# Optimization experiments

Hardware: AMD Instinct MI355X
Metric: run time of the kernel (lower is better)

The kernel has to match this reference:

```python
import jax, jax.numpy as jnp
import numpy as np

B, T, DIN = 1024, 256, 128
UNITS, OUT = 512, 64
INTER, CMD, MOTOR = 269, 179, 64  # AutoNCP(512, 64) layer split
SENS_FANOUT, INTER_FANOUT, MOTOR_FANIN = 134, 89, 89
LAYER_DIMS = [(DIN, INTER), (INTER, CMD), (CMD, MOTOR)]


def _layer_mask(rng, n_in, n_h, fanout=None, fanin=None):
    # sparse prev-layer -> layer block, dense recurrent block (ncps WiredCfCCell)
    m = np.zeros((n_in, n_h), dtype=bool)
    if fanout is not None:
        for i in range(n_in):
            m[i, rng.choice(n_h, size=fanout, replace=False)] = True
    else:
        for j in range(n_h):
            m[rng.choice(n_in, size=fanin, replace=False), j] = True
    full = np.concatenate([m, np.ones((n_h, n_h), dtype=bool)], axis=0)
    return jnp.asarray(full.T)  # (n_h, n_in + n_h): Linear weight layout


def setup_inputs() -> dict:
    key = jax.random.key(0)
    ks = jax.random.split(key, 30)
    rng = np.random.RandomState(22222)
    d = {}
    d["x"] = jax.random.normal(ks[0], (B, T, DIN), dtype=jnp.float32)
    d["hidden"] = jnp.zeros((B, UNITS), dtype=jnp.float32)
    d["mask0"] = _layer_mask(rng, DIN, INTER, fanout=SENS_FANOUT)
    d["mask1"] = _layer_mask(rng, INTER, CMD, fanout=INTER_FANOUT)
    d["mask2"] = _layer_mask(rng, CMD, MOTOR, fanin=MOTOR_FANIN)
    ki = 1
    for li, (n_in, n_h) in enumerate(LAYER_DIMS):
        cat = n_in + n_h
        s = 1.0 / float(np.sqrt(cat))
        for nm in ("ff1", "ff2", "ta", "tb"):
            d[f"{nm}_w{li}"] = jax.random.uniform(ks[ki], (n_h, cat), minval=-s, maxval=s, dtype=jnp.float32); ki += 1
            d[f"{nm}_b{li}"] = jax.random.uniform(ks[ki], (n_h,), minval=-s, maxval=s, dtype=jnp.float32); ki += 1
    sf = 1.0 / float(np.sqrt(MOTOR))
    d["fc_w"] = jax.random.uniform(ks[ki], (OUT, MOTOR), minval=-sf, maxval=sf, dtype=jnp.float32)
    d["fc_b"] = jax.random.uniform(ks[ki + 1], (OUT,), minval=-sf, maxval=sf, dtype=jnp.float32)
    return d


def _cfc_cell(inp, h, w1, b1, w2, b2, wa, ba, wb, bb):
    xc = jnp.concatenate([inp, h], axis=-1)
    ff1 = jnp.tanh(xc @ w1.T + b1)
    ff2 = jnp.tanh(xc @ w2.T + b2)
    ts = 1.0  # default elapsed time in CfC when no timespans given
    t_interp = jax.nn.sigmoid((xc @ wa.T + ba) * ts + (xc @ wb.T + bb))
    return ff1 * (1.0 - t_interp) + t_interp * ff2


def reference(x, hidden, mask0, mask1, mask2,
              ff1_w0, ff1_b0, ff2_w0, ff2_b0, ta_w0, ta_b0, tb_w0, tb_b0,
              ff1_w1, ff1_b1, ff2_w1, ff2_b1, ta_w1, ta_b1, tb_w1, tb_b1,
              ff1_w2, ff1_b2, ff2_w2, ff2_b2, ta_w2, ta_b2, tb_w2, tb_b2,
              fc_w, fc_b):
    m0 = mask0.astype(ff1_w0.dtype)
    m1 = mask1.astype(ff1_w1.dtype)
    m2 = mask2.astype(ff1_w2.dtype)
    layers = (
        (ff1_w0 * m0, ff1_b0, ff2_w0 * m0, ff2_b0, ta_w0, ta_b0, tb_w0, tb_b0),
        (ff1_w1 * m1, ff1_b1, ff2_w1 * m1, ff2_b1, ta_w1, ta_b1, tb_w1, tb_b1),
        (ff1_w2 * m2, ff1_b2, ff2_w2 * m2, ff2_b2, ta_w2, ta_b2, tb_w2, tb_b2),
    )
    h0 = hidden[:, :INTER]
    h1 = hidden[:, INTER:INTER + CMD]
    h2 = hidden[:, INTER + CMD:]

    def step(carry, xt):
        c0, c1, c2 = carry
        n0 = _cfc_cell(xt, c0, *layers[0])  # inter layer
        n1 = _cfc_cell(n0, c1, *layers[1])  # command layer
        n2 = _cfc_cell(n1, c2, *layers[2])  # motor layer
        return (n0, n1, n2), n2

    (f0, f1, f2), outs = jax.lax.scan(step, (h0, h1, h2), jnp.swapaxes(x, 0, 1))
    predictions = jnp.einsum('tbm,om->bto', outs, fc_w) + fc_b  # (B,T,OUT)
    hn = jnp.concatenate([f0, f1, f2], axis=-1)  # (B,UNITS)
    return predictions, hn
```

## Files before the change

kernel.cpp:

```cpp
#include <hip/hip_runtime.h>
#include <math.h>


namespace {
constexpr int kBatch = 1024;
constexpr int kT     = 256;
constexpr int kDIN   = 128;
constexpr int kUNITS = 512;
constexpr int kINTER = 269;
constexpr int kCMD   = 179;
constexpr int kMOTOR = 64;
constexpr int kOUT   = 64;

constexpr int kCAT0 = kDIN + kINTER;
constexpr int kCAT1 = kINTER + kCMD;
constexpr int kCAT2 = kCMD + kMOTOR;

constexpr int kC0r = 3 * kINTER;
constexpr int kC1r = 3 * kCMD;
constexpr int kC2r = 3 * kMOTOR;
constexpr int kC0p = 808;
constexpr int kC1p = 540;
constexpr int kC2p = 192;
constexpr int kP0 = 202;
constexpr int kP1 = 135;
constexpr int kP2 = 48;
constexpr int kK40 = 100;
constexpr int kK41 = 112;
constexpr int kK42 = 64;
constexpr int kS0 = kK40 * 4;
constexpr int kS1 = kK41 * 4;
constexpr int kS2 = kK42 * 4;

constexpr int kQ0 = kK40 * kC0p;
constexpr int kQ1 = kK41 * kC1p;
constexpr int kQ2 = kK42 * kC2p;
constexpr int kQ  = kQ0 + kQ1 + kQ2;
constexpr int kBCN = kC0p + kC1p + kC2p;
constexpr int kBCOff = kQ * 4;

constexpr int kMT = 4;
constexpr int kNT = 768;

static_assert(kK40 % 4 == 0 && kK41 % 4 == 0 && kK42 % 4 == 0, "ping-pong");
static_assert(kC0p % 4 == 0 && kC1p % 4 == 0 && kC2p % 4 == 0, "4-col");
}

__device__ __forceinline__ int detect_mask_mode(const void* m0) {
  const unsigned int* w = (const unsigned int*)m0;
  if (w[32] == 0x01010101u && w[33] == 0x01010101u &&
      w[34] == 0x01010101u && w[35] == 0x01010101u)
    return 0;
  if (w[128] == 0x3F800000u && w[129] == 0x3F800000u && w[130] == 0x3F800000u)
    return 2;
  return 1;
}

__device__ __forceinline__ bool mask_at(const void* mk, int idx, int mode) {
  if (mode == 0) return ((const unsigned char*)mk)[idx] != 0;
  if (mode == 1) return ((const int*)mk)[idx] != 0;
  return ((const float*)mk)[idx] != 0.0f;
}

__global__ void prep_kernel(
    const void* __restrict__ m0_, const void* __restrict__ m1_,
    const void* __restrict__ m2_,
    const float* __restrict__ f1w0, const float* __restrict__ f2w0,
    const float* __restrict__ taw0, const float* __restrict__ tbw0,
    const float* __restrict__ f1w1, const float* __restrict__ f2w1,
    const float* __restrict__ taw1, const float* __restrict__ tbw1,
    const float* __restrict__ f1w2, const float* __restrict__ f2w2,
    const float* __restrict__ taw2, const float* __restrict__ tbw2,
    const float* __restrict__ f1b0, const float* __restrict__ f2b0,
    const float* __restrict__ tab0, const float* __restrict__ tbb0,
    const float* __restrict__ f1b1, const float* __restrict__ f2b1,
    const float* __restrict__ tab1, const float* __restrict__ tbb1,
    const float* __restrict__ f1b2, const float* __restrict__ f2b2,
    const float* __restrict__ tab2, const float* __restrict__ tbb2,
    float* __restrict__ ws) {
  int i = blockIdx.x * 256 + threadIdx.x;
  const int mode = detect_mask_mode(m0_);
  if (i < kQ) {
    int qi, NCp, ncols, cat, nh, baseq;
    const void* mk;
    const float *wf1, *wf2, *wta, *wtb;
    if (i < kQ0) {
      qi = i; NCp = kC0p; ncols = kC0r; cat = kCAT0; nh = kINTER; mk = m0_;
      wf1 = f1w0; wf2 = f2w0; wta = taw0; wtb = tbw0; baseq = 0;
    } else if (i < kQ0 + kQ1) {
      qi = i - kQ0; NCp = kC1p; ncols = kC1r; cat = kCAT1; nh = kCMD; mk = m1_;
      wf1 = f1w1; wf2 = f2w1; wta = taw1; wtb = tbw1; baseq = kQ0;
    } else {
      qi = i - kQ0 - kQ1; NCp = kC2p; ncols = kC2r; cat = kCAT2; nh = kMOTOR;
      mk = m2_;
      wf1 = f1w2; wf2 = f2w2; wta = taw2; wtb = tbw2; baseq = kQ0 + kQ1;
    }
    int k4 = qi / NCp;
    int j  = qi % NCp;
    float v[4] = {0.0f, 0.0f, 0.0f, 0.0f};
    if (j < ncols) {
#pragma unroll
      for (int kk = 0; kk < 4; ++kk) {
        int k = k4 * 4 + kk;
        float r = 0.0f;
        if (k < cat) {
          if (j < nh) {
            r = mask_at(mk, j * cat + k, mode) ? wf1[j * cat + k] : 0.0f;
          } else if (j < 2 * nh) {
            int jj = j - nh;
            r = mask_at(mk, jj * cat + k, mode) ? wf2[jj * cat + k] : 0.0f;
          } else {
            int jj = j - 2 * nh;
            r = wta[jj * cat + k] + wtb[jj * cat + k];
          }
        }
        v[kk] = r;
      }
    }
    ((float4*)ws)[baseq + qi] = make_float4(v[0], v[1], v[2], v[3]);
  } else if (i < kQ + kBCN) {
    int pos = i - kQ;
    int j = pos;
    int nh, ncols;
    const float *bf1, *bf2, *bta, *btb;
    if (j < kC0p) {
      nh = kINTER; ncols = kC0r;
      bf1 = f1b0; bf2 = f2b0; bta = tab0; btb = tbb0;
    } else if (j < kC0p + kC1p) {
      j -= kC0p; nh = kCMD; ncols = kC1r;
      bf1 = f1b1; bf2 = f2b1; bta = tab1; btb = tbb1;
    } else {
      j -= kC0p + kC1p; nh = kMOTOR; ncols = kC2r;
      bf1 = f1b2; bf2 = f2b2; bta = tab2; btb = tbb2;
    }
    float r = 0.0f;
    if (j < ncols) {
      if (j < nh) r = bf1[j];
      else if (j < 2 * nh) r = bf2[j - nh];
      else r = bta[j - 2 * nh] + btb[j - 2 * nh];
    }
    ws[kBCOff + pos] = r;
  }
}

template <int AST>
__device__ __forceinline__ void fma4(const float4 (&w)[4],
                                     const float* __restrict__ ak,
                                     float (&acc)[4][kMT]) {
#pragma unroll
  for (int r = 0; r < kMT; ++r) {
    float4 av = *(const float4*)(ak + r * AST);
#pragma unroll
    for (int c = 0; c < 4; ++c) {
      acc[c][r] = fmaf(w[c].x, av.x, acc[c][r]);
      acc[c][r] = fmaf(w[c].y, av.y, acc[c][r]);
      acc[c][r] = fmaf(w[c].z, av.z, acc[c][r]);
      acc[c][r] = fmaf(w[c].w, av.w, acc[c][r]);
    }
  }
}

template <int NK4, int NCOLS, int AST, int PST>
__device__ __forceinline__ void mv4(const float4* __restrict__ wp,
                                    const float* __restrict__ a,
                                    float* __restrict__ pc,
                                    const float* __restrict__ bias,
                                    int j) {
  constexpr int P = NCOLS / 4;
  const float4* pw = wp + j;
  float acc[4][kMT];
#pragma unroll
  for (int c = 0; c < 4; ++c) {
    const float b = bias[c * P + j];
#pragma unroll
    for (int r = 0; r < kMT; ++r) acc[c][r] = b;
  }
  float4 U0[4], U1[4], V0[4], V1[4];
#pragma unroll
  for (int c = 0; c < 4; ++c) {
    U0[c] = pw[0 * NCOLS + c * P];
    U1[c] = pw[1 * NCOLS + c * P];
    V0[c] = pw[2 * NCOLS + c * P];
    V1[c] = pw[3 * NCOLS + c * P];
  }
  const float* ak = a;
#pragma unroll 1
  for (int k4 = 0; k4 + 8 <= NK4; k4 += 4) {
    fma4<AST>(U0, ak, acc);
    fma4<AST>(U1, ak + 4, acc);
#pragma unroll
    for (int c = 0; c < 4; ++c) {
      U0[c] = pw[(k4 + 4) * NCOLS + c * P];
      U1[c] = pw[(k4 + 5) * NCOLS + c * P];
    }
    fma4<AST>(V0, ak + 8, acc);
    fma4<AST>(V1, ak + 12, acc);
#pragma unroll
    for (int c = 0; c < 4; ++c) {
      V0[c] = pw[(k4 + 6) * NCOLS + c * P];
      V1[c] = pw[(k4 + 7) * NCOLS + c * P];
    }
    ak += 16;
  }
  fma4<AST>(U0, ak, acc);
  fma4<AST>(U1, ak + 4, acc);
  fma4<AST>(V0, ak + 8, acc);
  fma4<AST>(V1, ak + 12, acc);
#pragma unroll
  for (int r = 0; r < kMT; ++r)
#pragma unroll
    for (int c = 0; c < 4; ++c) pc[r * PST + c * P + j] = acc[c][r];
}

__device__ __forceinline__ float cfc_combine(float p1, float p2, float pt) {
  float f1 = tanhf(p1);
  float f2 = tanhf(p2);
  float ti = 1.0f / (1.0f + expf(-pt));
  return f1 + ti * (f2 - f1);
}

__global__ __launch_bounds__(kNT) void ncp_main(
    const float* __restrict__ x, const float* __restrict__ hidden,
    const float* __restrict__ ws, const float* __restrict__ fcw,
    const float* __restrict__ fcb, float* __restrict__ out) {
  __shared__ __align__(16) float xc0[kMT][kS0];
  __shared__ __align__(16) float xc1[kMT][kS1];
  __shared__ __align__(16) float xc2[kMT][kS2];
  __shared__ __align__(16) float pa0[kMT][kC0p];
  __shared__ __align__(16) float pa1[kMT][kC1p];
  __shared__ __align__(16) float pa2[kMT][kC2p];
  __shared__ float s_fcwT[64 * 64];
  __shared__ float s_bc[kBCN];
  __shared__ float s_fcb[64];

  const int tid = threadIdx.x;
  const int b0 = blockIdx.x * kMT;

#pragma unroll
  for (int r = 0; r < kMT; ++r) {
    if (tid < kS0) xc0[r][tid] = 0.0f;
    if (tid < kS1) xc1[r][tid] = 0.0f;
    if (tid < kS2) xc2[r][tid] = 0.0f;
  }
  __syncthreads();
  for (int i = tid; i < kMT * kUNITS; i += kNT) {
    int r = i >> 9, u = i & 511;
    float v = hidden[(size_t)(b0 + r) * kUNITS + u];
    if (u < kINTER) xc0[r][kDIN + u] = v;
    else if (u < kINTER + kCMD) xc1[r][u] = v;
    else xc2[r][kCMD + (u - (kINTER + kCMD))] = v;
  }
  for (int i = tid; i < kBCN; i += kNT) s_bc[i] = ws[kBCOff + i];
  if (tid < 64) s_fcb[tid] = fcb[tid];
  for (int i = tid; i < 64 * 64; i += kNT) {
    int m = i >> 6, o = i & 63;
    s_fcwT[i] = fcw[o * 64 + m];
  }
  if (tid < 128) {
    int r = tid >> 5, d4 = tid & 31;
    *(float4*)&xc0[r][d4 * 4] =
        *(const float4*)&x[(size_t)(b0 + r) * (kT * kDIN) + d4 * 4];
  }
  __syncthreads();

  const float4* wp0 = (const float4*)ws;
  const float4* wp1 = wp0 + kQ0;
  const float4* wp2 = wp1 + kQ1;

  for (int p = 0; p < kT + 3; ++p) {
    if (tid < 256) {
      if (p < kT && tid < kP0)
        mv4<kK40, kC0p, kS0, kC0p>(wp0, &xc0[0][0], &pa0[0][0], s_bc, tid);
    } else if (tid < 448) {
      const int pi = tid - 256;
      if (p >= 1 && p <= kT && pi < kP1)
        mv4<kK41, kC1p, kS1, kC1p>(wp1, &xc1[0][0], &pa1[0][0], s_bc + kC0p,
                                   pi);
    } else if (tid < 512) {
      const int pi = tid - 448;
      if (p >= 2 && p <= kT + 1 && pi < kP2)
        mv4<kK42, kC2p, kS2, kC2p>(wp2, &xc2[0][0], &pa2[0][0],
                                   s_bc + kC0p + kC1p, pi);
    } else if (tid >= 704) {
      if (p >= 3) {
        const int o = tid - 704;
        const int t_fc = p - 3;
        float a0 = s_fcb[o], a1 = a0, a2 = a0, a3 = a0;
        for (int m = 0; m < kMOTOR; ++m) {
          float w = s_fcwT[m * 64 + o];
          a0 = fmaf(xc2[0][kCMD + m], w, a0);
          a1 = fmaf(xc2[1][kCMD + m], w, a1);
          a2 = fmaf(xc2[2][kCMD + m], w, a2);
          a3 = fmaf(xc2[3][kCMD + m], w, a3);
        }
        size_t base =
            (size_t)b0 * (kT * kOUT) + (size_t)t_fc * kOUT + o;
        const size_t rstride = (size_t)kT * kOUT;
        out[base] = a0;
        out[base + rstride] = a1;
        out[base + 2 * rstride] = a2;
        out[base + 3 * rstride] = a3;
      }
    }
    __syncthreads();
    if (tid < kINTER) {
      if (p < kT) {
#pragma unroll
        for (int r = 0; r < kMT; ++r) {
          float v = cfc_combine(pa0[r][tid], pa0[r][tid + kINTER],
                                pa0[r][tid + 2 * kINTER]);
          xc1[r][tid] = v;
          xc0[r][kDIN + tid] = v;
        }
      }
    } else if (tid >= 320 && tid < 320 + kCMD) {
      if (p >= 1 && p <= kT) {
        const int j = tid - 320;
#pragma unroll
        for (int r = 0; r < kMT; ++r) {
          float v = cfc_combine(pa1[r][j], pa1[r][j + kCMD],
                                pa1[r][j + 2 * kCMD]);
          xc2[r][j] = v;
          xc1[r][kINTER + j] = v;
        }
      }
    } else if (tid >= 512 && tid < 512 + kMOTOR) {
      if (p >= 2 && p <= kT + 1) {
        const int j = tid - 512;
#pragma unroll
        for (int r = 0; r < kMT; ++r) {
          float v = cfc_combine(pa2[r][j], pa2[r][j + kMOTOR],
                                pa2[r][j + 2 * kMOTOR]);
          xc2[r][kCMD + j] = v;
        }
      }
    } else if (tid >= 576 && tid < 704) {
      if (p + 1 < kT) {
        const int i2 = tid - 576;
        const int r = i2 >> 5, d4 = i2 & 31;
        *(float4*)&xc0[r][d4 * 4] =
            *(const float4*)&x[(size_t)(b0 + r) * (kT * kDIN) +
                               (size_t)(p + 1) * kDIN + d4 * 4];
      }
    }
    __syncthreads();
  }

  const size_t hnoff = (size_t)kBatch * kT * kOUT;
  for (int i = tid; i < kMT * kUNITS; i += kNT) {
    int r = i >> 9, u = i & 511;
    float v;
    if (u < kINTER) v = xc0[r][kDIN + u];
    else if (u < kINTER + kCMD) v = xc1[r][u];
    else v = xc2[r][kCMD + (u - (kINTER + kCMD))];
    out[hnoff + (size_t)(b0 + r) * kUNITS + u] = v;
  }
}

extern "C" void kernel_launch(void* const* d_in, const int* in_sizes, int n_in,
                              void* d_out, int out_size, void* d_ws, size_t ws_size,
                              hipStream_t stream) {
  (void)in_sizes; (void)n_in; (void)out_size; (void)ws_size;
  const float* x = (const float*)d_in[0];
  const float* hidden = (const float*)d_in[1];
  const void* m0 = d_in[2];
  const void* m1 = d_in[3];
  const void* m2 = d_in[4];
  const float* f1w0 = (const float*)d_in[5];
  const float* f1b0 = (const float*)d_in[6];
  const float* f2w0 = (const float*)d_in[7];
  const float* f2b0 = (const float*)d_in[8];
  const float* taw0 = (const float*)d_in[9];
  const float* tab0 = (const float*)d_in[10];
  const float* tbw0 = (const float*)d_in[11];
  const float* tbb0 = (const float*)d_in[12];
  const float* f1w1 = (const float*)d_in[13];
  const float* f1b1 = (const float*)d_in[14];
  const float* f2w1 = (const float*)d_in[15];
  const float* f2b1 = (const float*)d_in[16];
  const float* taw1 = (const float*)d_in[17];
  const float* tab1 = (const float*)d_in[18];
  const float* tbw1 = (const float*)d_in[19];
  const float* tbb1 = (const float*)d_in[20];
  const float* f1w2 = (const float*)d_in[21];
  const float* f1b2 = (const float*)d_in[22];
  const float* f2w2 = (const float*)d_in[23];
  const float* f2b2 = (const float*)d_in[24];
  const float* taw2 = (const float*)d_in[25];
  const float* tab2 = (const float*)d_in[26];
  const float* tbw2 = (const float*)d_in[27];
  const float* tbb2 = (const float*)d_in[28];
  const float* fcw = (const float*)d_in[29];
  const float* fcb = (const float*)d_in[30];
  float* ws = (float*)d_ws;
  float* out = (float*)d_out;

  const int prep_items = kQ + kBCN;
  prep_kernel<<<(prep_items + 255) / 256, 256, 0, stream>>>(
      m0, m1, m2,
      f1w0, f2w0, taw0, tbw0,
      f1w1, f2w1, taw1, tbw1,
      f1w2, f2w2, taw2, tbw2,
      f1b0, f2b0, tab0, tbb0,
      f1b1, f2b1, tab1, tbb1,
      f1b2, f2b2, tab2, tbb2,
      ws);

  ncp_main<<<kBatch / kMT, kNT, 0, stream>>>(x, hidden, ws, fcw, fcb, out);
}
```

Before: 8.416 ms.

## Prefetch weights across steps, register-stage activations, spread combine over more threads

The first four weight k-rows are now loaded into registers once before the time loop and re-prefetched at the end of each matvec, so the first loads of the next step overlap the barrier and combine phase. Activation float4 loads from shared memory are staged into registers ahead of their FMAs. The per-element CfC combine is redistributed over 640 threads, one (column,row) pair each, instead of one thread per column looping over four rows. The x-row prefetch moves to the remaining 128 threads. launch_bounds gains a min-blocks hint of 3, which tightens the register budget and may cause spills given the extra live weight and activation registers.

Result: slower. 22.60 ms (+168.6%).

```diff
diff --git a/kernel.cpp b/kernel.cpp
--- a/kernel.cpp
+++ b/kernel.cpp
@@ -42,7 +42,12 @@
 constexpr int kMT = 4;
 constexpr int kNT = 768;
 
-static_assert(kK40 % 4 == 0 && kK41 % 4 == 0 && kK42 % 4 == 0, "ping-pong");
+constexpr int kJ0 = kINTER * kMT;
+constexpr int kJ1 = kJ0 + kCMD * kMT;
+constexpr int kJ2 = kJ1 + kMOTOR * kMT;
+constexpr int kCW = 640;
+
+static_assert(kK40 % 4 == 0 && kK41 % 4 == 0 && kK42 % 4 == 0, "pipeline");
 static_assert(kC0p % 4 == 0 && kC1p % 4 == 0 && kC2p % 4 == 0, "4-col");
 }
 
@@ -143,31 +148,38 @@
   }
 }
 
-template <int AST>
-__device__ __forceinline__ void fma4(const float4 (&w)[4],
-                                     const float* __restrict__ ak,
-                                     float (&acc)[4][kMT]) {
+template <int NCOLS>
+__device__ __forceinline__ void wload4(const float4* __restrict__ pw,
+                                       float4 (&W)[4], int k4) {
+  constexpr int P = NCOLS / 4;
+#pragma unroll
+  for (int c = 0; c < 4; ++c) W[c] = pw[k4 * NCOLS + c * P];
+}
+
+__device__ __forceinline__ void fma4r(const float4 (&w)[4],
+                                      const float4 (&av)[kMT],
+                                      float (&acc)[4][kMT]) {
 #pragma unroll
   for (int r = 0; r < kMT; ++r) {
-    float4 av = *(const float4*)(ak + r * AST);
 #pragma unroll
     for (int c = 0; c < 4; ++c) {
-      acc[c][r] = fmaf(w[c].x, av.x, acc[c][r]);
-      acc[c][r] = fmaf(w[c].y, av.y, acc[c][r]);
-      acc[c][r] = fmaf(w[c].z, av.z, acc[c][r]);
-      acc[c][r] = fmaf(w[c].w, av.w, acc[c][r]);
+      acc[c][r] = fmaf(w[c].x, av[r].x, acc[c][r]);
+      acc[c][r] = fmaf(w[c].y, av[r].y, acc[c][r]);
+      acc[c][r] = fmaf(w[c].z, av[r].z, acc[c][r]);
+      acc[c][r] = fmaf(w[c].w, av[r].w, acc[c][r]);
     }
   }
 }
 
 template <int NK4, int NCOLS, int AST, int PST>
-__device__ __forceinline__ void mv4(const float4* __restrict__ wp,
+__device__ __forceinline__ void mv4(const float4* __restrict__ pw,
                                     const float* __restrict__ a,
                                     float* __restrict__ pc,
                                     const float* __restrict__ bias,
-                                    int j) {
+                                    int j,
+                                    float4 (&U0)[4], float4 (&U1)[4],
+                                    float4 (&V0)[4], float4 (&V1)[4]) {
   constexpr int P = NCOLS / 4;
-  const float4* pw = wp + j;
   float acc[4][kMT];
 #pragma unroll
   for (int c = 0; c < 4; ++c) {
@@ -175,41 +187,52 @@
 #pragma unroll
     for (int r = 0; r < kMT; ++r) acc[c][r] = b;
   }
-  float4 U0[4], U1[4], V0[4], V1[4];
-#pragma unroll
-  for (int c = 0; c < 4; ++c) {
-    U0[c] = pw[0 * NCOLS + c * P];
-    U1[c] = pw[1 * NCOLS + c * P];
-    V0[c] = pw[2 * NCOLS + c * P];
-    V1[c] = pw[3 * NCOLS + c * P];
+  float4 A0[kMT], A1[kMT], B0[kMT], B1[kMT];
+#pragma unroll
+  for (int r = 0; r < kMT; ++r) {
+    A0[r] = *(const float4*)(a + r * AST + 0);
+    A1[r] = *(const float4*)(a + r * AST + 4);
   }
   const float* ak = a;
 #pragma unroll 1
   for (int k4 = 0; k4 + 8 <= NK4; k4 += 4) {
-    fma4<AST>(U0, ak, acc);
-    fma4<AST>(U1, ak + 4, acc);
-#pragma unroll
-    for (int c = 0; c < 4; ++c) {
-      U0[c] = pw[(k4 + 4) * NCOLS + c * P];
-      U1[c] = pw[(k4 + 5) * NCOLS + c * P];
-    }
-    fma4<AST>(V0, ak + 8, acc);
-    fma4<AST>(V1, ak + 12, acc);
-#pragma unroll
-    for (int c = 0; c < 4; ++c) {
-      V0[c] = pw[(k4 + 6) * NCOLS + c * P];
-      V1[c] = pw[(k4 + 7) * NCOLS + c * P];
-    }
+#pragma unroll
+    for (int r = 0; r < kMT; ++r) {
+      B0[r] = *(const float4*)(ak + r * AST + 8);
+      B1[r] = *(const float4*)(ak + r * AST + 12);
+    }
+    fma4r(U0, A0, acc);
+    fma4r(U1, A1, acc);
+    wload4<NCOLS>(pw, U0, k4 + 4);
+    wload4<NCOLS>(pw, U1, k4 + 5);
+#pragma unroll
+    for (int r = 0; r < kMT; ++r) {
+      A0[r] = *(const float4*)(ak + r * AST + 16);
+      A1[r] = *(const float4*)(ak + r * AST + 20);
+    }
+    fma4r(V0, B0, acc);
+    fma4r(V1, B1, acc);
+    wload4<NCOLS>(pw, V0, k4 + 6);
+    wload4<NCOLS>(pw, V1, k4 + 7);
     ak += 16;
   }
-  fma4<AST>(U0, ak, acc);
-  fma4<AST>(U1, ak + 4, acc);
-  fma4<AST>(V0, ak + 8, acc);
-  fma4<AST>(V1, ak + 12, acc);
+#pragma unroll
+  for (int r = 0; r < kMT; ++r) {
+    B0[r] = *(const float4*)(ak + r * AST + 8);
+    B1[r] = *(const float4*)(ak + r * AST + 12);
+  }
+  fma4r(U0, A0, acc);
+  fma4r(U1, A1, acc);
+  fma4r(V0, B0, acc);
+  fma4r(V1, B1, acc);
 #pragma unroll
   for (int r = 0; r < kMT; ++r)
 #pragma unroll
     for (int c = 0; c < 4; ++c) pc[r * PST + c * P + j] = acc[c][r];
+  wload4<NCOLS>(pw, U0, 0);
+  wload4<NCOLS>(pw, U1, 1);
+  wload4<NCOLS>(pw, V0, 2);
+  wload4<NCOLS>(pw, V1, 3);
 }
 
 __device__ __forceinline__ float cfc_combine(float p1, float p2, float pt) {
@@ -219,7 +242,7 @@
   return f1 + ti * (f2 - f1);
 }
 
-__global__ __launch_bounds__(kNT) void ncp_main(
+__global__ __launch_bounds__(kNT, 3) void ncp_main(
     const float* __restrict__ x, const float* __restrict__ hidden,
     const float* __restrict__ ws, const float* __restrict__ fcw,
     const float* __restrict__ fcb, float* __restrict__ out) {
@@ -261,26 +284,42 @@
     *(float4*)&xc0[r][d4 * 4] =
         *(const float4*)&x[(size_t)(b0 + r) * (kT * kDIN) + d4 * 4];
   }
-  __syncthreads();
 
   const float4* wp0 = (const float4*)ws;
   const float4* wp1 = wp0 + kQ0;
   const float4* wp2 = wp1 + kQ1;
 
+  float4 U0[4], U1[4], V0[4], V1[4];
+  if (tid < kP0) {
+    const float4* pw = wp0 + tid;
+    wload4<kC0p>(pw, U0, 0); wload4<kC0p>(pw, U1, 1);
+    wload4<kC0p>(pw, V0, 2); wload4<kC0p>(pw, V1, 3);
+  } else if (tid >= 256 && tid < 256 + kP1) {
+    const float4* pw = wp1 + (tid - 256);
+    wload4<kC1p>(pw, U0, 0); wload4<kC1p>(pw, U1, 1);
+    wload4<kC1p>(pw, V0, 2); wload4<kC1p>(pw, V1, 3);
+  } else if (tid >= 448 && tid < 448 + kP2) {
+    const float4* pw = wp2 + (tid - 448);
+    wload4<kC2p>(pw, U0, 0); wload4<kC2p>(pw, U1, 1);
+    wload4<kC2p>(pw, V0, 2); wload4<kC2p>(pw, V1, 3);
+  }
+  __syncthreads();
+
   for (int p = 0; p < kT + 3; ++p) {
     if (tid < 256) {
       if (p < kT && tid < kP0)
-        mv4<kK40, kC0p, kS0, kC0p>(wp0, &xc0[0][0], &pa0[0][0], s_bc, tid);
+        mv4<kK40, kC0p, kS0, kC0p>(wp0 + tid, &xc0[0][0], &pa0[0][0], s_bc,
+                                   tid, U0, U1, V0, V1);
     } else if (tid < 448) {
       const int pi = tid - 256;
       if (p >= 1 && p <= kT && pi < kP1)
-        mv4<kK41, kC1p, kS1, kC1p>(wp1, &xc1[0][0], &pa1[0][0], s_bc + kC0p,
-                                   pi);
+        mv4<kK41, kC1p, kS1, kC1p>(wp1 + pi, &xc1[0][0], &pa1[0][0],
+                                   s_bc + kC0p, pi, U0, U1, V0, V1);
     } else if (tid < 512) {
       const int pi = tid - 448;
       if (p >= 2 && p <= kT + 1 && pi < kP2)
-        mv4<kK42, kC2p, kS2, kC2p>(wp2, &xc2[0][0], &pa2[0][0],
-                                   s_bc + kC0p + kC1p, pi);
+        mv4<kK42, kC2p, kS2, kC2p>(wp2 + pi, &xc2[0][0], &pa2[0][0],
+                                   s_bc + kC0p + kC1p, pi, U0, U1, V0, V1);
     } else if (tid >= 704) {
       if (p >= 3) {
         const int o = tid - 704;
@@ -303,40 +342,38 @@
       }
     }
     __syncthreads();
-    if (tid < kINTER) {
-      if (p < kT) {
-#pragma unroll
-        for (int r = 0; r < kMT; ++r) {
-          float v = cfc_combine(pa0[r][tid], pa0[r][tid + kINTER],
-                                pa0[r][tid + 2 * kINTER]);
-          xc1[r][tid] = v;
-          xc0[r][kDIN + tid] = v;
+    if (tid < kCW) {
+      for (int g = tid; g < kJ2; g += kCW) {
+        if (g < kJ0) {
+          if (p < kT) {
+            const int col = g >> 2, r = g & 3;
+            float v = cfc_combine(pa0[r][col], pa0[r][col + kINTER],
+                                  pa0[r][col + 2 * kINTER]);
+            xc1[r][col] = v;
+            xc0[r][kDIN + col] = v;
+          }
+        } else if (g < kJ1) {
+          if (p >= 1 && p <= kT) {
+            const int gg = g - kJ0;
+            const int col = gg >> 2, r = gg & 3;
+            float v = cfc_combine(pa1[r][col], pa1[r][col + kCMD],
+                                  pa1[r][col + 2 * kCMD]);
+            xc2[r][col] = v;
+            xc1[r][kINTER + col] = v;
+          }
+        } else {
+          if (p >= 2 && p <= kT + 1) {
+            const int gg = g - kJ1;
+            const int col = gg >> 2, r = gg & 3;
+            float v = cfc_combine(pa2[r][col], pa2[r][col + kMOTOR],
+                                  pa2[r][col + 2 * kMOTOR]);
+            xc2[r][kCMD + col] = v;
+          }
         }
       }
-    } else if (tid >= 320 && tid < 320 + kCMD) {
-      if (p >= 1 && p <= kT) {
-        const int j = tid - 320;
-#pragma unroll
-        for (int r = 0; r < kMT; ++r) {
-          float v = cfc_combine(pa1[r][j], pa1[r][j + kCMD],
-                                pa1[r][j + 2 * kCMD]);
-          xc2[r][j] = v;
-          xc1[r][kINTER + j] = v;
-        }
-      }
-    } else if (tid >= 512 && tid < 512 + kMOTOR) {
-      if (p >= 2 && p <= kT + 1) {
-        const int j = tid - 512;
-#pragma unroll
-        for (int r = 0; r < kMT; ++r) {
-          float v = cfc_combine(pa2[r][j], pa2[r][j + kMOTOR],
-                                pa2[r][j + 2 * kMOTOR]);
-          xc2[r][kCMD + j] = v;
-        }
-      }
-    } else if (tid >= 576 && tid < 704) {
+    } else {
       if (p + 1 < kT) {
-        const int i2 = tid - 576;
+        const int i2 = tid - kCW;
         const int r = i2 >> 5, d4 = i2 & 31;
         *(float4*)&xc0[r][d4 * 4] =
             *(const float4*)&x[(size_t)(b0 + r) * (kT * kDIN) +
```

## Assign one thread per hidden unit computing all three gates with fused CfC combine

Applied to the files above, without the earlier changes.

Reorganizes the packed weight layout so each thread owns one hidden unit and computes its ff1, ff2 and time-gate pre-activations together, then applies the CfC combine in registers. This removes the shared-memory pre-activation buffers and the separate combine pass that reread them, and trims padding columns. The block shrinks from 768 to 640 threads, so x-prefetch threads now load two vectors each. Per-thread work becomes 3 columns instead of 4, and the activation loads are hoisted into registers with double buffering.

Measured after the change: 7.771 ms. 1.08x faster.

```diff
diff --git a/kernel.cpp b/kernel.cpp
--- a/kernel.cpp
+++ b/kernel.cpp
@@ -16,34 +16,25 @@
 constexpr int kCAT1 = kINTER + kCMD;
 constexpr int kCAT2 = kCMD + kMOTOR;
 
-constexpr int kC0r = 3 * kINTER;
-constexpr int kC1r = 3 * kCMD;
-constexpr int kC2r = 3 * kMOTOR;
-constexpr int kC0p = 808;
-constexpr int kC1p = 540;
-constexpr int kC2p = 192;
-constexpr int kP0 = 202;
-constexpr int kP1 = 135;
-constexpr int kP2 = 48;
-constexpr int kK40 = 100;
-constexpr int kK41 = 112;
-constexpr int kK42 = 64;
-constexpr int kS0 = kK40 * 4;
-constexpr int kS1 = kK41 * 4;
-constexpr int kS2 = kK42 * 4;
-
-constexpr int kQ0 = kK40 * kC0p;
-constexpr int kQ1 = kK41 * kC1p;
-constexpr int kQ2 = kK42 * kC2p;
+constexpr int kNK40 = 100;
+constexpr int kNK41 = 112;
+constexpr int kNK42 = 61;
+constexpr int kS0 = 400;
+constexpr int kS1 = 448;
+constexpr int kS2 = 256;
+
+constexpr int kQ0 = kNK40 * 3 * kINTER;
+constexpr int kQ1 = kNK41 * 3 * kCMD;
+constexpr int kQ2 = kNK42 * 3 * kMOTOR;
 constexpr int kQ  = kQ0 + kQ1 + kQ2;
-constexpr int kBCN = kC0p + kC1p + kC2p;
+constexpr int kB0 = 3 * kINTER;
+constexpr int kB1 = 3 * kCMD;
+constexpr int kB2 = 3 * kMOTOR;
+constexpr int kBCN = kB0 + kB1 + kB2;
 constexpr int kBCOff = kQ * 4;
 
 constexpr int kMT = 4;
-constexpr int kNT = 768;
-
-static_assert(kK40 % 4 == 0 && kK41 % 4 == 0 && kK42 % 4 == 0, "ping-pong");
-static_assert(kC0p % 4 == 0 && kC1p % 4 == 0 && kC2p % 4 == 0, "4-col");
+constexpr int kNT = 640;
 }
 
 __device__ __forceinline__ int detect_mask_mode(const void* m0) {
@@ -81,135 +72,74 @@
   int i = blockIdx.x * 256 + threadIdx.x;
   const int mode = detect_mask_mode(m0_);
   if (i < kQ) {
-    int qi, NCp, ncols, cat, nh, baseq;
+    int qi, nh, cat, baseq;
     const void* mk;
     const float *wf1, *wf2, *wta, *wtb;
     if (i < kQ0) {
-      qi = i; NCp = kC0p; ncols = kC0r; cat = kCAT0; nh = kINTER; mk = m0_;
+      qi = i; nh = kINTER; cat = kCAT0; mk = m0_;
       wf1 = f1w0; wf2 = f2w0; wta = taw0; wtb = tbw0; baseq = 0;
     } else if (i < kQ0 + kQ1) {
-      qi = i - kQ0; NCp = kC1p; ncols = kC1r; cat = kCAT1; nh = kCMD; mk = m1_;
+      qi = i - kQ0; nh = kCMD; cat = kCAT1; mk = m1_;
       wf1 = f1w1; wf2 = f2w1; wta = taw1; wtb = tbw1; baseq = kQ0;
     } else {
-      qi = i - kQ0 - kQ1; NCp = kC2p; ncols = kC2r; cat = kCAT2; nh = kMOTOR;
-      mk = m2_;
+      qi = i - kQ0 - kQ1; nh = kMOTOR; cat = kCAT2; mk = m2_;
       wf1 = f1w2; wf2 = f2w2; wta = taw2; wtb = tbw2; baseq = kQ0 + kQ1;
     }
-    int k4 = qi / NCp;
-    int j  = qi % NCp;
-    float v[4] = {0.0f, 0.0f, 0.0f, 0.0f};
-    if (j < ncols) {
-#pragma unroll
-      for (int kk = 0; kk < 4; ++kk) {
-        int k = k4 * 4 + kk;
-        float r = 0.0f;
-        if (k < cat) {
-          if (j < nh) {
-            r = mask_at(mk, j * cat + k, mode) ? wf1[j * cat + k] : 0.0f;
-          } else if (j < 2 * nh) {
-            int jj = j - nh;
-            r = mask_at(mk, jj * cat + k, mode) ? wf2[jj * cat + k] : 0.0f;
-          } else {
-            int jj = j - 2 * nh;
-            r = wta[jj * cat + k] + wtb[jj * cat + k];
-          }
-        }
-        v[kk] = r;
-      }
+    const int k4  = qi / (3 * nh);
+    const int rem = qi % (3 * nh);
+    const int c   = rem / nh;
+    const int u   = rem % nh;
+    float v[4];
+#pragma unroll
+    for (int kk = 0; kk < 4; ++kk) {
+      const int k = k4 * 4 + kk;
+      float r = 0.0f;
+      if (k < cat) {
+        if (c == 0) {
+          r = mask_at(mk, u * cat + k, mode) ? wf1[u * cat + k] : 0.0f;
+        } else if (c == 1) {
+          r = mask_at(mk, u * cat + k, mode) ? wf2[u * cat + k] : 0.0f;
+        } else {
+          r = wta[u * cat + k] + wtb[u * cat + k];
+        }
+      }
+      v[kk] = r;
     }
     ((float4*)ws)[baseq + qi] = make_float4(v[0], v[1], v[2], v[3]);
   } else if (i < kQ + kBCN) {
-    int pos = i - kQ;
-    int j = pos;
-    int nh, ncols;
+    int j = i - kQ;
+    int nh;
     const float *bf1, *bf2, *bta, *btb;
-    if (j < kC0p) {
-      nh = kINTER; ncols = kC0r;
-      bf1 = f1b0; bf2 = f2b0; bta = tab0; btb = tbb0;
-    } else if (j < kC0p + kC1p) {
-      j -= kC0p; nh = kCMD; ncols = kC1r;
-      bf1 = f1b1; bf2 = f2b1; bta = tab1; btb = tbb1;
+    if (j < kB0) {
+      nh = kINTER; bf1 = f1b0; bf2 = f2b0; bta = tab0; btb = tbb0;
+    } else if (j < kB0 + kB1) {
+      j -= kB0; nh = kCMD; bf1 = f1b1; bf2 = f2b1; bta = tab1; btb = tbb1;
     } else {
-      j -= kC0p + kC1p; nh = kMOTOR; ncols = kC2r;
-      bf1 = f1b2; bf2 = f2b2; bta = tab2; btb = tbb2;
-    }
-    float r = 0.0f;
-    if (j < ncols) {
-      if (j < nh) r = bf1[j];
-      else if (j < 2 * nh) r = bf2[j - nh];
-      else r = bta[j - 2 * nh] + btb[j - 2 * nh];
-    }
-    ws[kBCOff + pos] = r;
-  }
-}
-
-template <int AST>
-__device__ __forceinline__ void fma4(const float4 (&w)[4],
-                                     const float* __restrict__ ak,
-                                     float (&acc)[4][kMT]) {
+      j -= kB0 + kB1; nh = kMOTOR; bf1 = f1b2; bf2 = f2b2; bta = tab2;
+      btb = tbb2;
+    }
+    const int c = j / nh, u = j % nh;
+    float r;
+    if (c == 0) r = bf1[u];
+    else if (c == 1) r = bf2[u];
+    else r = bta[u] + btb[u];
+    ws[kBCOff + (i - kQ)] = r;
+  }
+}
+
+__device__ __forceinline__ void fma3(const float4 (&w)[3],
+                                     const float4 (&av)[kMT],
+                                     float (&acc)[3][kMT]) {
 #pragma unroll
   for (int r = 0; r < kMT; ++r) {
-    float4 av = *(const float4*)(ak + r * AST);
-#pragma unroll
-    for (int c = 0; c < 4; ++c) {
-      acc[c][r] = fmaf(w[c].x, av.x, acc[c][r]);
-      acc[c][r] = fmaf(w[c].y, av.y, acc[c][r]);
-      acc[c][r] = fmaf(w[c].z, av.z, acc[c][r]);
-      acc[c][r] = fmaf(w[c].w, av.w, acc[c][r]);
-    }
-  }
-}
-
-template <int NK4, int NCOLS, int AST, int PST>
-__device__ __forceinline__ void mv4(const float4* __restrict__ wp,
-                                    const float* __restrict__ a,
-                                    float* __restrict__ pc,
-                                    const float* __restrict__ bias,
-                                    int j) {
-  constexpr int P = NCOLS / 4;
-  const float4* pw = wp + j;
-  float acc[4][kMT];
-#pragma unroll
-  for (int c = 0; c < 4; ++c) {
-    const float b = bias[c * P + j];
-#pragma unroll
-    for (int r = 0; r < kMT; ++r) acc[c][r] = b;
-  }
-  float4 U0[4], U1[4], V0[4], V1[4];
-#pragma unroll
-  for (int c = 0; c < 4; ++c) {
-    U0[c] = pw[0 * NCOLS + c * P];
-    U1[c] = pw[1 * NCOLS + c * P];
-    V0[c] = pw[2 * NCOLS + c * P];
-    V1[c] = pw[3 * NCOLS + c * P];
-  }
-  const float* ak = a;
-#pragma unroll 1
-  for (int k4 = 0; k4 + 8 <= NK4; k4 += 4) {
-    fma4<AST>(U0, ak, acc);
-    fma4<AST>(U1, ak + 4, acc);
-#pragma unroll
-    for (int c = 0; c < 4; ++c) {
-      U0[c] = pw[(k4 + 4) * NCOLS + c * P];
-      U1[c] = pw[(k4 + 5) * NCOLS + c * P];
-    }
-    fma4<AST>(V0, ak + 8, acc);
-    fma4<AST>(V1, ak + 12, acc);
-#pragma unroll
-    for (int c = 0; c < 4; ++c) {
-      V0[c] = pw[(k4 + 6) * NCOLS + c * P];
-      V1[c] = pw[(k4 + 7) * NCOLS + c * P];
-    }
-    ak += 16;
-  }
-  fma4<AST>(U0, ak, acc);
-  fma4<AST>(U1, ak + 4, acc);
-  fma4<AST>(V0, ak + 8, acc);
-  fma4<AST>(V1, ak + 12, acc);
-#pragma unroll
-  for (int r = 0; r < kMT; ++r)
-#pragma unroll
-    for (int c = 0; c < 4; ++c) pc[r * PST + c * P + j] = acc[c][r];
+#pragma unroll
+    for (int c = 0; c < 3; ++c) {
+      acc[c][r] = fmaf(w[c].x, av[r].x, acc[c][r]);
+      acc[c][r] = fmaf(w[c].y, av[r].y, acc[c][r]);
+      acc[c][r] = fmaf(w[c].z, av[r].z, acc[c][r]);
+      acc[c][r] = fmaf(w[c].w, av[r].w, acc[c][r]);
+    }
+  }
 }
 
 __device__ __forceinline__ float cfc_combine(float p1, float p2, float pt) {
@@ -217,6 +147,63 @@
   float f2 = tanhf(p2);
   float ti = 1.0f / (1.0f + expf(-pt));
   return f1 + ti * (f2 - f1);
+}
+
+template <int NK4, int NH, int AST>
+__device__ __forceinline__ void mv3(const float4* __restrict__ pw,
+                                    const float* __restrict__ a,
+                                    const float* __restrict__ bias,
+                                    int u, float (&v)[kMT]) {
+  float acc[3][kMT];
+#pragma unroll
+  for (int c = 0; c < 3; ++c) {
+    const float b = bias[c * NH + u];
+#pragma unroll
+    for (int r = 0; r < kMT; ++r) acc[c][r] = b;
+  }
+  float4 W0[3], W1[3], a0[kMT], a1[kMT];
+#pragma unroll
+  for (int c = 0; c < 3; ++c) {
+    W0[c] = pw[(0 * 3 + c) * NH];
+    W1[c] = pw[(1 * 3 + c) * NH];
+  }
+#pragma unroll
+  for (int r = 0; r < kMT; ++r) {
+    a0[r] = *(const float4*)(a + r * AST + 0);
+    a1[r] = *(const float4*)(a + r * AST + 4);
+  }
+  int k4 = 0;
+#pragma unroll 1
+  for (; k4 + 3 < NK4; k4 += 2) {
+    fma3(W0, a0, acc);
+#pragma unroll
+    for (int c = 0; c < 3; ++c) W0[c] = pw[((k4 + 2) * 3 + c) * NH];
+#pragma unroll
+    for (int r = 0; r < kMT; ++r)
+      a0[r] = *(const float4*)(a + r * AST + (k4 + 2) * 4);
+    fma3(W1, a1, acc);
+#pragma unroll
+    for (int c = 0; c < 3; ++c) W1[c] = pw[((k4 + 3) * 3 + c) * NH];
+#pragma unroll
+    for (int r = 0; r < kMT; ++r)
+      a1[r] = *(const float4*)(a + r * AST + (k4 + 3) * 4);
+  }
+  if constexpr (NK4 % 2 == 0) {
+    fma3(W0, a0, acc);
+    fma3(W1, a1, acc);
+  } else {
+    fma3(W0, a0, acc);
+#pragma unroll
+    for (int c = 0; c < 3; ++c) W0[c] = pw[((k4 + 2) * 3 + c) * NH];
+#pragma unroll
+    for (int r = 0; r < kMT; ++r)
+      a0[r] = *(const float4*)(a + r * AST + (k4 + 2) * 4);
+    fma3(W1, a1, acc);
+    fma3(W0, a0, acc);
+  }
+#pragma unroll
+  for (int r = 0; r < kMT; ++r)
+    v[r] = cfc_combine(acc[0][r], acc[1][r], acc[2][r]);
 }
 
 __global__ __launch_bounds__(kNT) void ncp_main(
@@ -226,9 +213,6 @@
   __shared__ __align__(16) float xc0[kMT][kS0];
   __shared__ __align__(16) float xc1[kMT][kS1];
   __shared__ __align__(16) float xc2[kMT][kS2];
-  __shared__ __align__(16) float pa0[kMT][kC0p];
-  __shared__ __align__(16) float pa1[kMT][kC1p];
-  __shared__ __align__(16) float pa2[kMT][kC2p];
   __shared__ float s_fcwT[64 * 64];
   __shared__ float s_bc[kBCN];
   __shared__ float s_fcb[64];
@@ -268,22 +252,21 @@
   const float4* wp2 = wp1 + kQ1;
 
   for (int p = 0; p < kT + 3; ++p) {
-    if (tid < 256) {
-      if (p < kT && tid < kP0)
-        mv4<kK40, kC0p, kS0, kC0p>(wp0, &xc0[0][0], &pa0[0][0], s_bc, tid);
-    } else if (tid < 448) {
-      const int pi = tid - 256;
-      if (p >= 1 && p <= kT && pi < kP1)
-        mv4<kK41, kC1p, kS1, kC1p>(wp1, &xc1[0][0], &pa1[0][0], s_bc + kC0p,
-                                   pi);
+    float v[kMT];
+    if (tid < 320) {
+      if (p < kT && tid < kINTER)
+        mv3<kNK40, kINTER, kS0>(wp0 + tid, &xc0[0][0], s_bc, tid, v);
     } else if (tid < 512) {
-      const int pi = tid - 448;
-      if (p >= 2 && p <= kT + 1 && pi < kP2)
-        mv4<kK42, kC2p, kS2, kC2p>(wp2, &xc2[0][0], &pa2[0][0],
-                                   s_bc + kC0p + kC1p, pi);
-    } else if (tid >= 704) {
+      const int u = tid - 320;
+      if (p >= 1 && p <= kT && u < kCMD)
+        mv3<kNK41, kCMD, kS1>(wp1 + u, &xc1[0][0], s_bc + kB0, u, v);
+    } else if (tid < 576) {
+      const int u = tid - 512;
+      if (p >= 2 && p <= kT + 1)
+        mv3<kNK42, kMOTOR, kS2>(wp2 + u, &xc2[0][0], s_bc + kB0 + kB1, u, v);
+    } else {
       if (p >= 3) {
-        const int o = tid - 704;
+        const int o = tid - 576;
         const int t_fc = p - 3;
         float a0 = s_fcb[o], a1 = a0, a2 = a0, a3 = a0;
         for (int m = 0; m < kMOTOR; ++m) {
@@ -293,8 +276,7 @@
           a2 = fmaf(xc2[2][kCMD + m], w, a2);
           a3 = fmaf(xc2[3][kCMD + m], w, a3);
         }
-        size_t base =
-            (size_t)b0 * (kT * kOUT) + (size_t)t_fc * kOUT + o;
+        size_t base = (size_t)b0 * (kT * kOUT) + (size_t)t_fc * kOUT + o;
         const size_t rstride = (size_t)kT * kOUT;
         out[base] = a0;
         out[base + rstride] = a1;
@@ -303,44 +285,41 @@
       }
     }
     __syncthreads();
-    if (tid < kINTER) {
-      if (p < kT) {
+    if (tid < 320) {
+      if (p < kT && tid < kINTER) {
 #pragma unroll
         for (int r = 0; r < kMT; ++r) {
-          float v = cfc_combine(pa0[r][tid], pa0[r][tid + kINTER],
-                                pa0[r][tid + 2 * kINTER]);
-          xc1[r][tid] = v;
-          xc0[r][kDIN + tid] = v;
-        }
-      }
-    } else if (tid >= 320 && tid < 320 + kCMD) {
-      if (p >= 1 && p <= kT) {
-        const int j = tid - 320;
+          xc1[r][tid] = v[r];
+          xc0[r][kDIN + tid] = v[r];
+        }
+      }
+    } else if (tid < 512) {
+      const int u = tid - 320;
+      if (p >= 1 && p <= kT && u < kCMD) {
 #pragma unroll
         for (int r = 0; r < kMT; ++r) {
-          float v = cfc_combine(pa1[r][j], pa1[r][j + kCMD],
-                                pa1[r][j + 2 * kCMD]);
-          xc2[r][j] = v;
-          xc1[r][kINTER + j] = v;
-        }
-      }
-    } else if (tid >= 512 && tid < 512 + kMOTOR) {
+          xc2[r][u] = v[r];
+          xc1[r][kINTER + u] = v[r];
+        }
+      }
+    } else if (tid < 576) {
+      const int u = tid - 512;
       if (p >= 2 && p <= kT + 1) {
-        const int j = tid - 512;
-#pragma unroll
-        for (int r = 0; r < kMT; ++r) {
-          float v = cfc_combine(pa2[r][j], pa2[r][j + kMOTOR],
-                                pa2[r][j + 2 * kMOTOR]);
-          xc2[r][kCMD + j] = v;
-        }
-      }
-    } else if (tid >= 576 && tid < 704) {
+#pragma unroll
+        for (int r = 0; r < kMT; ++r)
+          xc2[r][kCMD + u] = v[r];
+      }
+    } else {
       if (p + 1 < kT) {
         const int i2 = tid - 576;
-        const int r = i2 >> 5, d4 = i2 & 31;
-        *(float4*)&xc0[r][d4 * 4] =
-            *(const float4*)&x[(size_t)(b0 + r) * (kT * kDIN) +
-                               (size_t)(p + 1) * kDIN + d4 * 4];
+#pragma unroll
+        for (int q = 0; q < 2; ++q) {
+          const int idx = i2 + q * 64;
+          const int r = idx >> 5, d4 = idx & 31;
+          *(float4*)&xc0[r][d4 * 4] =
+              *(const float4*)&x[(size_t)(b0 + r) * (kT * kDIN) +
+                                 (size_t)(p + 1) * kDIN + d4 * 4];
+        }
       }
     }
     __syncthreads();
```
